# Performance work log

Hardware: AMD Instinct MI355X
Metric: run time of the kernel (lower is better)

The kernel has to match this reference:

```python
import jax, jax.numpy as jnp
import numpy as np

N_WIRES = 6
DIM = 1 << N_WIRES  # 64, equals input channel dim C for amplitude encoding
HID = N_WIRES       # hidden_dim = len(ops)


def _rx(theta):
    c = jnp.cos(theta / 2).astype(jnp.complex64)
    s = jnp.sin(theta / 2).astype(jnp.complex64)
    return jnp.stack([jnp.stack([c, -1j * s]), jnp.stack([-1j * s, c])])


def _ry(theta):
    c = jnp.cos(theta / 2).astype(jnp.complex64)
    s = jnp.sin(theta / 2).astype(jnp.complex64)
    return jnp.stack([jnp.stack([c, -s]), jnp.stack([s, c])])


def _apply_1q(state, U, wire):
    # state: (N, 2, 2, ..., 2); apply 2x2 U on qubit axis wire+1
    s = jnp.moveaxis(state, wire + 1, 1)
    s = jnp.einsum('ab,nb...->na...', U, s)
    return jnp.moveaxis(s, 1, wire + 1)


def _apply_cnot(state, c, t):
    # flip target axis where control bit == 1
    s = jnp.moveaxis(state, (c + 1, t + 1), (1, 2))
    s = jnp.concatenate([s[:, :1], jnp.flip(s[:, 1:2], axis=2)], axis=1)
    return jnp.moveaxis(s, (1, 2), (c + 1, t + 1))


def _expval_z(state, wire):
    # <Z_wire> = P(bit=0) - P(bit=1)
    p = state.real ** 2 + state.imag ** 2
    p = jnp.moveaxis(p, wire + 1, 1).reshape(p.shape[0], 2, -1)
    return p[:, 0].sum(-1) - p[:, 1].sum(-1)


def _value_layer(x_flat, params, qk):
    # amplitude encoding: normalize input into state amplitudes (C == DIM)
    norm = jnp.linalg.norm(x_flat, axis=-1, keepdims=True)
    psi = (x_flat / norm).astype(jnp.complex64)
    state = psi.reshape((x_flat.shape[0],) + (2,) * N_WIRES)
    rx0, ry0, ry1 = params[0], params[1], params[2]
    for j in range(N_WIRES):
        state = _apply_1q(state, _rx(rx0[j]), j)
        state = _apply_1q(state, _ry(ry0[j]), j)
    for j in range(N_WIRES):
        state = _apply_cnot(state, j, (j + 1) % N_WIRES)
    for j in range(N_WIRES):
        state = _apply_1q(state, _ry(ry1[j]), j)
    if qk:
        z0 = _expval_z(state, 0)
        return jnp.stack([z0] * HID, axis=-1)  # qk=True replicates wire-0 <Z>
    return jnp.stack([_expval_z(state, w) for w in range(N_WIRES)], axis=-1)


def setup_inputs() -> dict:
    key = jax.random.key(0)
    k1, k2, k3, k4 = jax.random.split(key, 4)
    B, T, C = 16, 2048, DIM
    return {
        'x': jax.random.normal(k1, (B, T, C), dtype=jnp.float32),
        'params_q': jax.random.normal(k2, (3, N_WIRES), dtype=jnp.float32),
        'params_k': jax.random.normal(k3, (3, N_WIRES), dtype=jnp.float32),
        'params_v': jax.random.normal(k4, (3, N_WIRES), dtype=jnp.float32),
    }


def reference(x, params_q, params_k, params_v):
    B, T, C = x.shape
    xf = x.reshape(B * T, C)
    q = _value_layer(xf, params_q, True).reshape(B, T, HID)
    k = _value_layer(xf, params_k, True).reshape(B, T, HID)
    v = _value_layer(xf, params_v, False).reshape(B, T, HID)
    scores = jnp.einsum('btd,bsd->bts', q, k) / jnp.sqrt(jnp.float32(HID))
    attn = jax.nn.softmax(scores, axis=-1)
    return jnp.einsum('bts,bsd->btd', attn, v)
```

## Files before the change

### kernel.cpp

```cpp
#include <hip/hip_runtime.h>
#include <math.h>

#define NWIRES 6
#define DIM 64
#define NTOK 32768
#define NBATCH 16
#define TPB 2048
#define NMOM 16
#define SQRT6F 2.4494897427831781f
#define CSTRIDE 160

__global__ void qsa_prep(const float* __restrict__ pq,
                         const float* __restrict__ pk,
                         const float* __restrict__ pv,
                         float* __restrict__ cs) {
    int b = threadIdx.x;
    for (int circ = 0; circ < 3; ++circ) {
        const float* p = (circ == 0) ? pq : (circ == 1 ? pk : pv);
        float* T = cs + circ * CSTRIDE;
        float d = 0.f;
#pragma unroll
        for (int j = 0; j < 6; ++j)
            d += 0.5f * p[j] * ((b & (32 >> j)) ? -1.f : 1.f);
        float sd, cd;
        sincosf(d, &sd, &cd);
        T[b] = cd;
        T[64 + b] = sd;
        if (b < 12) {
            float s, c;
            sincosf(0.5f * p[6 + b], &s, &c);
            T[128 + b * 2 + 0] = c;
            T[128 + b * 2 + 1] = s;
        }
    }
}

template<int M>
__device__ __forceinline__ void whad(float* v) {
#pragma unroll
    for (int i = 0; i < DIM; ++i) {
        if (i & M) continue;
        int j = i | M;
        float a = v[i], b = v[j];
        v[i] = a + b;
        v[j] = a - b;
    }
}

template<int M>
__device__ __forceinline__ void ryr(float* v, float c, float s) {
#pragma unroll
    for (int i = 0; i < DIM; ++i) {
        if (i & M) continue;
        int j = i | M;
        float a = v[i], b = v[j];
        v[i] = c * a - s * b;
        v[j] = s * a + c * b;
    }
}

template<int MC, int MT>
__device__ __forceinline__ void cnr(float* v) {
#pragma unroll
    for (int i = 0; i < DIM; ++i) {
        if (!(i & MC) || (i & MT)) continue;
        int j = i | MT;
        float t = v[i]; v[i] = v[j]; v[j] = t;
    }
}

__global__ __attribute__((amdgpu_waves_per_eu(3, 3)))
__launch_bounds__(64) void qsa_sim(
        const float* __restrict__ x,
        const float* __restrict__ cs,
        float* __restrict__ zq,
        float* __restrict__ kv) {
    int g = blockIdx.x * 64 + threadIdx.x;
    int par = g & 1;
    int token = g >> 1;
    int circ = blockIdx.y;
    const float* T = cs + circ * CSTRIDE;
    const float* P = T + 128;

    float v[DIM];
    const float4* xp4 = (const float4*)(x + (size_t)token * DIM);
#pragma unroll
    for (int k = 0; k < DIM / 4; ++k) {
        float4 q = xp4[k];
        v[4*k+0] = q.x; v[4*k+1] = q.y; v[4*k+2] = q.z; v[4*k+3] = q.w;
    }

    whad<32>(v); whad<16>(v); whad<8>(v); whad<4>(v); whad<2>(v); whad<1>(v);
    const float4* tp4 = (const float4*)(T + par * 64);
#pragma unroll
    for (int k = 0; k < DIM / 4; ++k) {
        float4 q = tp4[k];
        v[4*k+0] *= q.x; v[4*k+1] *= q.y; v[4*k+2] *= q.z; v[4*k+3] *= q.w;
    }
    whad<32>(v); whad<16>(v); whad<8>(v); whad<4>(v); whad<2>(v); whad<1>(v);

    ryr<32>(v, P[0],  P[1]);
    ryr<16>(v, P[2],  P[3]);
    ryr< 8>(v, P[4],  P[5]);
    ryr< 4>(v, P[6],  P[7]);
    ryr< 2>(v, P[8],  P[9]);
    ryr< 1>(v, P[10], P[11]);
    cnr<32,16>(v);
    cnr<16, 8>(v);
    cnr< 8, 4>(v);
    cnr< 4, 2>(v);
    cnr< 2, 1>(v);
    cnr< 1,32>(v);
    ryr<32>(v, P[12], P[13]);
    ryr<16>(v, P[14], P[15]);
    ryr< 8>(v, P[16], P[17]);
    ryr< 4>(v, P[18], P[19]);
    ryr< 2>(v, P[20], P[21]);
    ryr< 1>(v, P[22], P[23]);

    if (circ < 2) {
        float nl = 0.f, s0 = 0.f;
#pragma unroll
        for (int i = 0; i < DIM; ++i) {
            float p2 = v[i] * v[i];
            nl += p2;
            if (!(i & 32)) s0 += p2;
        }
        float norm2 = nl + __shfl_xor(nl, 1, 64);
        float S0 = s0 + __shfl_xor(s0, 1, 64);
        float z0 = (2.f * S0 - norm2) / norm2;
        if (par == 0) {
            if (circ == 0) zq[token] = SQRT6F * z0;
            else           kv[(size_t)token * 8] = z0;
        }
    } else {
        float nl = 0.f, s0=0.f, s1=0.f, s2=0.f, s3=0.f, s4=0.f, s5=0.f;
#pragma unroll
        for (int i = 0; i < DIM; ++i) {
            float p2 = v[i] * v[i];
            nl += p2;
            if (!(i & 32)) s0 += p2;
            if (!(i & 16)) s1 += p2;
            if (!(i &  8)) s2 += p2;
            if (!(i &  4)) s3 += p2;
            if (!(i &  2)) s4 += p2;
            if (!(i &  1)) s5 += p2;
        }
        float norm2 = nl + __shfl_xor(nl, 1, 64);
        float S0 = s0 + __shfl_xor(s0, 1, 64);
        float S1 = s1 + __shfl_xor(s1, 1, 64);
        float S2 = s2 + __shfl_xor(s2, 1, 64);
        float S3 = s3 + __shfl_xor(s3, 1, 64);
        float S4 = s4 + __shfl_xor(s4, 1, 64);
        float S5 = s5 + __shfl_xor(s5, 1, 64);
        float inv = 1.0f / norm2;
        float* o = kv + (size_t)token * 8;
        if (par == 0) {
            o[1] = (2.f*S0 - norm2) * inv;
            o[2] = (2.f*S1 - norm2) * inv;
            o[3] = (2.f*S2 - norm2) * inv;
        } else {
            o[4] = (2.f*S3 - norm2) * inv;
            o[5] = (2.f*S4 - norm2) * inv;
            o[6] = (2.f*S5 - norm2) * inv;
        }
    }
}

__global__ __attribute__((amdgpu_waves_per_eu(1, 2)))
__launch_bounds__(64) void qsa_moments_partial(
        const float* __restrict__ kv,
        float* __restrict__ mpart) {
    int blk = blockIdx.x;
    int b = blk >> 3, c = blk & 7;
    int lane = threadIdx.x;
    float S[NMOM], H[NMOM][6];
#pragma unroll
    for (int m = 0; m < NMOM; ++m) {
        S[m] = 0.f;
#pragma unroll
        for (int w = 0; w < 6; ++w) H[m][w] = 0.f;
    }
    const float* base = kv + ((size_t)(b * TPB + c * 256)) * 8;
#pragma unroll
    for (int r = 0; r < 4; ++r) {
        const float4* e = (const float4*)(base + (size_t)(r * 64 + lane) * 8);
        float4 e0 = e[0], e1 = e[1];
        float z = e0.x;
        float v0 = e0.y, v1 = e0.z, v2 = e0.w, v3 = e1.x, v4 = e1.y, v5 = e1.z;
        float pw = 1.f;
#pragma unroll
        for (int m = 0; m < NMOM; ++m) {
            S[m] += pw;
            H[m][0] += pw * v0; H[m][1] += pw * v1; H[m][2] += pw * v2;
            H[m][3] += pw * v3; H[m][4] += pw * v4; H[m][5] += pw * v5;
            pw *= z;
        }
    }
#pragma unroll
    for (int d = 32; d >= 1; d >>= 1) {
#pragma unroll
        for (int m = 0; m < NMOM; ++m) {
            S[m] += __shfl_xor(S[m], d, 64);
#pragma unroll
            for (int w = 0; w < 6; ++w) H[m][w] += __shfl_xor(H[m][w], d, 64);
        }
    }
    if (lane == 0) {
        float* o = mpart + (size_t)blk * 112;
#pragma unroll
        for (int m = 0; m < NMOM; ++m) {
            float* om = o + m * 7;
            om[0] = S[m];
            om[1] = H[m][0]; om[2] = H[m][1]; om[3] = H[m][2];
            om[4] = H[m][3]; om[5] = H[m][4]; om[6] = H[m][5];
        }
    }
}

__global__ __launch_bounds__(256) void qsa_eval(
        const float* __restrict__ zq,
        const float* __restrict__ mpart,
        float* __restrict__ out) {
    __shared__ float sm[112];
    int bk = blockIdx.x;
    int b = bk >> 3;
    int tid = threadIdx.x;
    if (tid < 112) {
        float s = 0.f;
#pragma unroll
        for (int c = 0; c < 8; ++c) s += mpart[(size_t)(b * 8 + c) * 112 + tid];
        sm[tid] = s;
    }
    __syncthreads();

    int t = bk * 256 + tid;
    float a = zq[t];
    float den = 0.f, o0 = 0.f, o1 = 0.f, o2 = 0.f, o3 = 0.f, o4 = 0.f, o5 = 0.f;
    float pw = 1.f;
#pragma unroll
    for (int m = 0; m < NMOM; ++m) {
        const float* mm = sm + m * 7;
        den += pw * mm[0];
        o0 += pw * mm[1]; o1 += pw * mm[2]; o2 += pw * mm[3];
        o3 += pw * mm[4]; o4 += pw * mm[5]; o5 += pw * mm[6];
        pw *= a * (1.0f / (m + 1));
    }
    float inv = 1.0f / den;
    float* o = out + (size_t)t * 6;
    float2* o2p = (float2*)o;
    o2p[0] = make_float2(o0 * inv, o1 * inv);
    o2p[1] = make_float2(o2 * inv, o3 * inv);
    o2p[2] = make_float2(o4 * inv, o5 * inv);
}

extern "C" void kernel_launch(void* const* d_in, const int* in_sizes, int n_in,
                              void* d_out, int out_size, void* d_ws, size_t ws_size,
                              hipStream_t stream) {
    const float* x  = (const float*)d_in[0];
    const float* pq = (const float*)d_in[1];
    const float* pk = (const float*)d_in[2];
    const float* pv = (const float*)d_in[3];
    float* w = (float*)d_ws;
    float* cs    = w;
    float* zq    = w + 512;
    float* kv    = w + 512 + NTOK;
    float* mpart = w + 512 + NTOK + NTOK * 8;
    float* out   = (float*)d_out;

    qsa_prep<<<1, 64, 0, stream>>>(pq, pk, pv, cs);
    qsa_sim<<<dim3(NTOK * 2 / 64, 3), 64, 0, stream>>>(x, cs, zq, kv);
    qsa_moments_partial<<<NBATCH * 8, 64, 0, stream>>>(kv, mpart);
    qsa_eval<<<NTOK / 256, 256, 0, stream>>>(zq, mpart, out);
}
```

Before: 94.69 us.

## Precompute fused circuit matrices and apply them as matvecs per token

The RX/RY/CNOT circuit after the Hadamard-diagonal-Hadamard stage is folded into precomputed 64x64 cosine and sine matrices, built by a new qsa_prepM kernel. qsa_sim now runs one thread per token instead of two: it applies one Walsh-Hadamard transform and then dense matvecs against those matrices, reading matrix rows from global or cache. The circuit arithmetic per token is no longer repeated, but each token now does about 64x64x2 FMAs, or half that for q/k where only 32 rows are needed. This is more arithmetic and more memory reads than the butterfly network, and it also halves the thread count.

```diff
diff --git a/kernel.cpp b/kernel.cpp
--- a/kernel.cpp
+++ b/kernel.cpp
@@ -36,18 +36,6 @@
 }
 
 template<int M>
-__device__ __forceinline__ void whad(float* v) {
-#pragma unroll
-    for (int i = 0; i < DIM; ++i) {
-        if (i & M) continue;
-        int j = i | M;
-        float a = v[i], b = v[j];
-        v[i] = a + b;
-        v[j] = a - b;
-    }
-}
-
-template<int M>
 __device__ __forceinline__ void ryr(float* v, float c, float s) {
 #pragma unroll
     for (int i = 0; i < DIM; ++i) {
@@ -69,101 +57,131 @@
     }
 }
 
-__global__ __attribute__((amdgpu_waves_per_eu(3, 3)))
+__global__ __attribute__((amdgpu_waves_per_eu(1, 1)))
+__launch_bounds__(64) void qsa_prepM(const float* __restrict__ cs,
+                                     float* __restrict__ Mmat) {
+    int c = blockIdx.x, b = threadIdx.x;
+    const float* T = cs + c * CSTRIDE;
+    const float* P = T + 128;
+    float st[DIM];
+#pragma unroll
+    for (int i = 0; i < DIM; ++i)
+        st[i] = (__popc(i & b) & 1) ? -1.f : 1.f;
+    ryr<32>(st, P[0],  P[1]);
+    ryr<16>(st, P[2],  P[3]);
+    ryr< 8>(st, P[4],  P[5]);
+    ryr< 4>(st, P[6],  P[7]);
+    ryr< 2>(st, P[8],  P[9]);
+    ryr< 1>(st, P[10], P[11]);
+    cnr<32,16>(st); cnr<16,8>(st); cnr<8,4>(st);
+    cnr<4,2>(st);   cnr<2,1>(st);  cnr<1,32>(st);
+    ryr<32>(st, P[12], P[13]);
+    ryr<16>(st, P[14], P[15]);
+    ryr< 8>(st, P[16], P[17]);
+    ryr< 4>(st, P[18], P[19]);
+    ryr< 2>(st, P[20], P[21]);
+    ryr< 1>(st, P[22], P[23]);
+    float cb = T[b], sb = T[64 + b];
+    float* Mc = Mmat + (size_t)c * 8192;
+    float* Ms = Mc + 4096;
+#pragma unroll
+    for (int r = 0; r < DIM; ++r) {
+        Mc[r * 64 + b] = st[r] * cb;
+        Ms[r * 64 + b] = st[r] * sb;
+    }
+}
+
+__global__ __attribute__((amdgpu_waves_per_eu(2, 2)))
 __launch_bounds__(64) void qsa_sim(
         const float* __restrict__ x,
-        const float* __restrict__ cs,
+        const float* __restrict__ Mmat,
         float* __restrict__ zq,
         float* __restrict__ kv) {
-    int g = blockIdx.x * 64 + threadIdx.x;
-    int par = g & 1;
-    int token = g >> 1;
+    int t = blockIdx.x * 64 + threadIdx.x;
     int circ = blockIdx.y;
-    const float* T = cs + circ * CSTRIDE;
-    const float* P = T + 128;
-
-    float v[DIM];
-    const float4* xp4 = (const float4*)(x + (size_t)token * DIM);
+    const float* Mc = Mmat + (size_t)circ * 8192;
+    const float* Ms = Mc + 4096;
+
+    float y[DIM];
+    const float4* xp4 = (const float4*)(x + (size_t)t * DIM);
 #pragma unroll
     for (int k = 0; k < DIM / 4; ++k) {
         float4 q = xp4[k];
-        v[4*k+0] = q.x; v[4*k+1] = q.y; v[4*k+2] = q.z; v[4*k+3] = q.w;
-    }
-
-    whad<32>(v); whad<16>(v); whad<8>(v); whad<4>(v); whad<2>(v); whad<1>(v);
-    const float4* tp4 = (const float4*)(T + par * 64);
-#pragma unroll
-    for (int k = 0; k < DIM / 4; ++k) {
-        float4 q = tp4[k];
-        v[4*k+0] *= q.x; v[4*k+1] *= q.y; v[4*k+2] *= q.z; v[4*k+3] *= q.w;
-    }
-    whad<32>(v); whad<16>(v); whad<8>(v); whad<4>(v); whad<2>(v); whad<1>(v);
-
-    ryr<32>(v, P[0],  P[1]);
-    ryr<16>(v, P[2],  P[3]);
-    ryr< 8>(v, P[4],  P[5]);
-    ryr< 4>(v, P[6],  P[7]);
-    ryr< 2>(v, P[8],  P[9]);
-    ryr< 1>(v, P[10], P[11]);
-    cnr<32,16>(v);
-    cnr<16, 8>(v);
-    cnr< 8, 4>(v);
-    cnr< 4, 2>(v);
-    cnr< 2, 1>(v);
-    cnr< 1,32>(v);
-    ryr<32>(v, P[12], P[13]);
-    ryr<16>(v, P[14], P[15]);
-    ryr< 8>(v, P[16], P[17]);
-    ryr< 4>(v, P[18], P[19]);
-    ryr< 2>(v, P[20], P[21]);
-    ryr< 1>(v, P[22], P[23]);
+        y[4*k+0] = q.x; y[4*k+1] = q.y; y[4*k+2] = q.z; y[4*k+3] = q.w;
+    }
+#pragma unroll
+    for (int M = 32; M >= 1; M >>= 1) {
+#pragma unroll
+        for (int i = 0; i < DIM; ++i) {
+            if (i & M) continue;
+            int j = i | M;
+            float a = y[i], b = y[j];
+            y[i] = a + b;
+            y[j] = a - b;
+        }
+    }
+    float n0 = 0.f, n1 = 0.f, n2 = 0.f, n3 = 0.f;
+#pragma unroll
+    for (int k = 0; k < DIM; k += 4) {
+        n0 += y[k]*y[k];   n1 += y[k+1]*y[k+1];
+        n2 += y[k+2]*y[k+2]; n3 += y[k+3]*y[k+3];
+    }
+    float n = 64.f * ((n0 + n1) + (n2 + n3));
+    float inv = 1.0f / n;
 
     if (circ < 2) {
-        float nl = 0.f, s0 = 0.f;
-#pragma unroll
-        for (int i = 0; i < DIM; ++i) {
-            float p2 = v[i] * v[i];
-            nl += p2;
-            if (!(i & 32)) s0 += p2;
-        }
-        float norm2 = nl + __shfl_xor(nl, 1, 64);
-        float S0 = s0 + __shfl_xor(s0, 1, 64);
-        float z0 = (2.f * S0 - norm2) / norm2;
-        if (par == 0) {
-            if (circ == 0) zq[token] = SQRT6F * z0;
-            else           kv[(size_t)token * 8] = z0;
-        }
+        float s0 = 0.f;
+#pragma unroll 1
+        for (int r = 0; r < 32; ++r) {
+            const float* cr = Mc + (r << 6);
+            const float* sr = Ms + (r << 6);
+            float c0=0.f,c1=0.f,c2=0.f,c3=0.f,d0=0.f,d1=0.f,d2=0.f,d3=0.f;
+#pragma unroll
+            for (int k = 0; k < DIM; k += 4) {
+                c0 += cr[k]  *y[k];   d0 += sr[k]  *y[k];
+                c1 += cr[k+1]*y[k+1]; d1 += sr[k+1]*y[k+1];
+                c2 += cr[k+2]*y[k+2]; d2 += sr[k+2]*y[k+2];
+                c3 += cr[k+3]*y[k+3]; d3 += sr[k+3]*y[k+3];
+            }
+            float dc = (c0 + c1) + (c2 + c3);
+            float ds = (d0 + d1) + (d2 + d3);
+            s0 += dc * dc + ds * ds;
+        }
+        float z0 = (2.f * s0 - n) * inv;
+        if (circ == 0) zq[t] = SQRT6F * z0;
+        else           kv[(size_t)t * 8] = z0;
     } else {
-        float nl = 0.f, s0=0.f, s1=0.f, s2=0.f, s3=0.f, s4=0.f, s5=0.f;
-#pragma unroll
-        for (int i = 0; i < DIM; ++i) {
-            float p2 = v[i] * v[i];
-            nl += p2;
-            if (!(i & 32)) s0 += p2;
-            if (!(i & 16)) s1 += p2;
-            if (!(i &  8)) s2 += p2;
-            if (!(i &  4)) s3 += p2;
-            if (!(i &  2)) s4 += p2;
-            if (!(i &  1)) s5 += p2;
-        }
-        float norm2 = nl + __shfl_xor(nl, 1, 64);
-        float S0 = s0 + __shfl_xor(s0, 1, 64);
-        float S1 = s1 + __shfl_xor(s1, 1, 64);
-        float S2 = s2 + __shfl_xor(s2, 1, 64);
-        float S3 = s3 + __shfl_xor(s3, 1, 64);
-        float S4 = s4 + __shfl_xor(s4, 1, 64);
-        float S5 = s5 + __shfl_xor(s5, 1, 64);
-        float inv = 1.0f / norm2;
-        float* o = kv + (size_t)token * 8;
-        if (par == 0) {
-            o[1] = (2.f*S0 - norm2) * inv;
-            o[2] = (2.f*S1 - norm2) * inv;
-            o[3] = (2.f*S2 - norm2) * inv;
-        } else {
-            o[4] = (2.f*S3 - norm2) * inv;
-            o[5] = (2.f*S4 - norm2) * inv;
-            o[6] = (2.f*S5 - norm2) * inv;
-        }
+        float a0=0.f,a1=0.f,a2=0.f,a3=0.f,a4=0.f,a5=0.f;
+#pragma unroll 1
+        for (int r = 0; r < 64; ++r) {
+            const float* cr = Mc + (r << 6);
+            const float* sr = Ms + (r << 6);
+            float c0=0.f,c1=0.f,c2=0.f,c3=0.f,d0=0.f,d1=0.f,d2=0.f,d3=0.f;
+#pragma unroll
+            for (int k = 0; k < DIM; k += 4) {
+                c0 += cr[k]  *y[k];   d0 += sr[k]  *y[k];
+                c1 += cr[k+1]*y[k+1]; d1 += sr[k+1]*y[k+1];
+                c2 += cr[k+2]*y[k+2]; d2 += sr[k+2]*y[k+2];
+                c3 += cr[k+3]*y[k+3]; d3 += sr[k+3]*y[k+3];
+            }
+            float dc = (c0 + c1) + (c2 + c3);
+            float ds = (d0 + d1) + (d2 + d3);
+            float p = dc * dc + ds * ds;
+            if (!(r & 32)) a0 += p;
+            if (!(r & 16)) a1 += p;
+            if (!(r &  8)) a2 += p;
+            if (!(r &  4)) a3 += p;
+            if (!(r &  2)) a4 += p;
+            if (!(r &  1)) a5 += p;
+        }
+        float* o = kv + (size_t)t * 8;
+        o[1] = (2.f*a0 - n) * inv;
+        o[2] = (2.f*a1 - n) * inv;
+        o[3] = (2.f*a2 - n) * inv;
+        o[4] = (2.f*a3 - n) * inv;
+        o[5] = (2.f*a4 - n) * inv;
+        o[6] = (2.f*a5 - n) * inv;
+        o[7] = 0.f;
     }
 }
 
@@ -263,13 +281,15 @@
     const float* pv = (const float*)d_in[3];
     float* w = (float*)d_ws;
     float* cs    = w;
-    float* zq    = w + 512;
-    float* kv    = w + 512 + NTOK;
-    float* mpart = w + 512 + NTOK + NTOK * 8;
+    float* Mmat  = w + 512;
+    float* zq    = Mmat + 3 * 8192;
+    float* kv    = zq + NTOK;
+    float* mpart = kv + NTOK * 8;
     float* out   = (float*)d_out;
 
     qsa_prep<<<1, 64, 0, stream>>>(pq, pk, pv, cs);
-    qsa_sim<<<dim3(NTOK * 2 / 64, 3), 64, 0, stream>>>(x, cs, zq, kv);
+    qsa_prepM<<<3, 64, 0, stream>>>(cs, Mmat);
+    qsa_sim<<<dim3(NTOK / 64, 3), 64, 0, stream>>>(x, Mmat, zq, kv);
     qsa_moments_partial<<<NBATCH * 8, 64, 0, stream>>>(kv, mpart);
     qsa_eval<<<NTOK / 256, 256, 0, stream>>>(zq, mpart, out);
 }
```

Result: slower. 151.0 us (+59.5%).
